# Optimization experiments

Hardware: AMD Instinct MI355X
Metric: run time of the kernel (lower is better)

## Reference

```python
import jax, jax.numpy as jnp
import numpy as np

N_NODES = 100000
N_FEAT = 512
HIDDEN = 128
N_CLASS = 16
N_EDGES = 3200000
ALPHA = 0.25
N_ITERS = 2


def setup_inputs() -> dict:
    key = jax.random.key(0)
    k1, k2, k3, k4, k5 = jax.random.split(key, 5)
    x = jax.random.normal(k1, (N_NODES, N_FEAT), dtype=jnp.float32)
    W1 = jax.random.normal(k2, (N_FEAT, HIDDEN), dtype=jnp.float32) * 0.05
    W2 = jax.random.normal(k3, (HIDDEN, N_CLASS), dtype=jnp.float32) * 0.05
    edge_src = jax.random.randint(k4, (N_EDGES,), 0, N_NODES, dtype=jnp.int32)
    edge_dst = jax.random.randint(k5, (N_EDGES,), 0, N_NODES, dtype=jnp.int32)
    return {"x": x, "W1": W1, "W2": W2, "edge_src": edge_src, "edge_dst": edge_dst}


def reference(x, W1, W2, edge_src, edge_dst):
    # 2-layer GCN features
    hidden_1 = jax.nn.relu(x @ W1)                       # [N, H]
    local_logits = hidden_1 @ W2                         # [N, C]
    # degree of each row of adj (unit edge weights)
    deg = jax.ops.segment_sum(
        jnp.ones_like(edge_src, dtype=x.dtype), edge_src, num_segments=N_NODES
    )                                                    # [N]
    scale = (1.0 - ALPHA) / jnp.maximum(deg, 1e-12)      # [N]
    logits = local_logits
    for _ in range(N_ITERS):
        # SpMM: (adj @ logits)[i] = sum_{(i,j) in E} logits[j]
        agg = jax.ops.segment_sum(logits[edge_dst], edge_src, num_segments=N_NODES)
        logits = scale[:, None] * agg + ALPHA * local_logits
    return jax.nn.log_softmax(logits, axis=1)
```

## Files before the change

### kernel.cpp

```cpp
#include <hip/hip_runtime.h>
#include <math.h>

#define N_NODES 100000
#define N_FEAT  512
#define HIDDEN  128
#define N_CLASS 16
#define N_EDGES 3200000
#define ALPHA   0.25f

#define NB   782
#define CAP  5120
#define TILE 8192
#define NTB  391

typedef __attribute__((ext_vector_type(8))) short short8;
typedef __attribute__((ext_vector_type(4))) float float4v;
typedef __attribute__((ext_vector_type(4))) unsigned uint4v;
typedef __attribute__((ext_vector_type(4))) int int4v;

__device__ inline short f2b(float f) {
    union { float f; unsigned u; } c; c.f = f;
    unsigned r = c.u + 0x7FFF + ((c.u >> 16) & 1);
    return (short)(r >> 16);
}

__device__ __forceinline__ void async_copy16(void* l, const void* g) {
    __builtin_amdgcn_global_load_lds(
        (const __attribute__((address_space(1))) void*)g,
        (__attribute__((address_space(3))) void*)l, 16, 0, 0);
}

__global__ void prep_kernel(const float* __restrict__ W1, const float* __restrict__ W2,
                            short* __restrict__ W1t, short* __restrict__ W2t,
                            int* __restrict__ cursor) {
    int t = blockIdx.x * 256 + threadIdx.x;
    if (t < N_FEAT * HIDDEN) {
        int k = t & 511, n = t >> 9;
        W1t[t] = f2b(W1[(size_t)k * HIDDEN + n]);
    }
    int t2 = t - N_FEAT * HIDDEN;
    if (t2 >= 0 && t2 < HIDDEN * N_CLASS) {
        int k = t2 & 127, n = t2 >> 7;
        W2t[t2] = f2b(W2[(size_t)k * N_CLASS + n]);
    }
    if (t < NB) cursor[t] = t * CAP;
}

__global__ __launch_bounds__(256) void mlp_mfma(const float* __restrict__ x,
                                                const short* __restrict__ W1t,
                                                const short* __restrict__ W2t,
                                                float* __restrict__ local_out,
                                                unsigned short* __restrict__ Lbf) {
    __shared__ __align__(16) char uS[34816];
    __shared__ __align__(16) short W2ts[16 * 136];

    float* const Asf = (float*)uS;
    short* const Bt  = (short*)(uS + 16384);
    short* const Hs  = (short*)uS;

    const int tid  = threadIdx.x;
    const int wave = tid >> 6;
    const int wl   = tid & 63;
    const int lane15 = wl & 15;
    const int quad   = wl >> 4;
    const long block_row = (long)blockIdx.x * 128;

    {
        int n = tid >> 4, koff = (tid & 15) * 8;
        *(short8*)&W2ts[n * 136 + koff] = *(const short8*)&W2t[n * 128 + koff];
    }

    float4v acc[4][4];
#pragma unroll
    for (int i = 0; i < 4; ++i)
#pragma unroll
        for (int j = 0; j < 4; ++j) acc[i][j] = (float4v){0.f, 0.f, 0.f, 0.f};

    const int wr0 = (wave >> 1) * 64;
    const int wc0 = (wave & 1) * 64;

    const int a_rsub = wl >> 3;
    const int a_cch  = (wl & 7) ^ a_rsub;
    const int b_rsub = wl >> 2;
    const int b_cch  = (wl & 3) ^ ((wl >> 3) & 3);
    char* const aBase = uS + wave * 4096;
    char* const bBase = uS + 16384 + wave * 2048;

    const int r7 = lane15 & 7;
    const int rb = (lane15 >> 1) & 3;

    for (int k0 = 0; k0 < N_FEAT; k0 += 32) {
#pragma unroll
        for (int c = 0; c < 4; ++c) {
            long gr = block_row + wave * 32 + c * 8 + a_rsub;
            if (gr > N_NODES - 1) gr = N_NODES - 1;
            async_copy16(aBase + c * 1024, x + gr * N_FEAT + k0 + a_cch * 4);
        }
#pragma unroll
        for (int c = 0; c < 2; ++c) {
            int rr = wave * 32 + c * 16 + b_rsub;
            async_copy16(bBase + c * 1024, W1t + rr * 512 + k0 + b_cch * 8);
        }
        __syncthreads();

        short8 af[4], bfr[4];
#pragma unroll
        for (int i = 0; i < 4; ++i) {
            const float* pa = Asf + (wr0 + i * 16 + lane15) * 32;
            float4 va = *(const float4*)(pa + (((2 * quad) ^ r7) << 2));
            float4 vb = *(const float4*)(pa + (((2 * quad + 1) ^ r7) << 2));
            short8 h;
            h[0] = f2b(va.x); h[1] = f2b(va.y); h[2] = f2b(va.z); h[3] = f2b(va.w);
            h[4] = f2b(vb.x); h[5] = f2b(vb.y); h[6] = f2b(vb.z); h[7] = f2b(vb.w);
            af[i] = h;
        }
#pragma unroll
        for (int j = 0; j < 4; ++j) {
            const short* pb = Bt + (wc0 + j * 16 + lane15) * 32;
            bfr[j] = *(const short8*)(pb + ((quad ^ rb) << 3));
        }
#pragma unroll
        for (int i = 0; i < 4; ++i)
#pragma unroll
            for (int j = 0; j < 4; ++j)
                acc[i][j] = __builtin_amdgcn_mfma_f32_16x16x32_bf16(af[i], bfr[j], acc[i][j], 0, 0, 0);
        __syncthreads();
    }

#pragma unroll
    for (int i = 0; i < 4; ++i)
#pragma unroll
        for (int j = 0; j < 4; ++j)
#pragma unroll
            for (int r = 0; r < 4; ++r) {
                int row = wr0 + i * 16 + quad * 4 + r;
                int colh = wc0 + j * 16 + lane15;
                Hs[row * 136 + colh] = f2b(fmaxf(acc[i][j][r], 0.f));
            }
    __syncthreads();

    float4v acc2[2];
    acc2[0] = (float4v){0.f, 0.f, 0.f, 0.f};
    acc2[1] = acc2[0];
#pragma unroll
    for (int ks = 0; ks < 4; ++ks) {
        short8 a0 = *(short8*)&Hs[(wave * 32 + lane15) * 136 + ks * 32 + quad * 8];
        short8 a1 = *(short8*)&Hs[(wave * 32 + 16 + lane15) * 136 + ks * 32 + quad * 8];
        short8 b  = *(short8*)&W2ts[lane15 * 136 + ks * 32 + quad * 8];
        acc2[0] = __builtin_amdgcn_mfma_f32_16x16x32_bf16(a0, b, acc2[0], 0, 0, 0);
        acc2[1] = __builtin_amdgcn_mfma_f32_16x16x32_bf16(a1, b, acc2[1], 0, 0, 0);
    }
#pragma unroll
    for (int i2 = 0; i2 < 2; ++i2)
#pragma unroll
        for (int r = 0; r < 4; ++r) {
            long grow = block_row + wave * 32 + i2 * 16 + quad * 4 + r;
            if (grow < N_NODES) {
                float v = acc2[i2][r];
                local_out[grow * N_CLASS + lane15] = v;
                Lbf[grow * N_CLASS + lane15] = (unsigned short)f2b(v);
            }
        }
}

__global__ __launch_bounds__(256) void partition_kernel(const int* __restrict__ src,
                                                        const int* __restrict__ dst,
                                                        int* __restrict__ cursor,
                                                        unsigned* __restrict__ bbuf) {
    __shared__ unsigned sbuf[TILE];
    __shared__ unsigned short sbkt[TILE];
    __shared__ int cnt[1024];
    __shared__ int off[1024];
    __shared__ int gbase[NB];
    __shared__ int psum[256];

    const int tid = threadIdx.x;
    const int e0 = blockIdx.x * TILE;
    int n = N_EDGES - e0; if (n > TILE) n = TILE;

    for (int i = tid; i < 1024; i += 256) cnt[i] = 0;
    __syncthreads();

    unsigned pk[32]; int br[32];
#pragma unroll
    for (int k = 0; k < 8; ++k) {
        int i0 = k * 1024 + tid * 4;
        if (i0 < n) {
            int4v s4 = __builtin_nontemporal_load((const int4v*)&src[e0 + i0]);
            int4v d4 = __builtin_nontemporal_load((const int4v*)&dst[e0 + i0]);
#pragma unroll
            for (int j = 0; j < 4; ++j) {
                int s = s4[j], d = d4[j];
                int b = s >> 7;
                int r = atomicAdd(&cnt[b], 1);
                pk[k * 4 + j] = ((unsigned)(s & 127) << 17) | (unsigned)d;
                br[k * 4 + j] = (b << 13) | r;
            }
        } else {
#pragma unroll
            for (int j = 0; j < 4; ++j) br[k * 4 + j] = -1;
        }
    }
    __syncthreads();

    int b4 = tid * 4;
    int c0 = cnt[b4], c1 = cnt[b4 + 1], c2 = cnt[b4 + 2], c3 = cnt[b4 + 3];
    int tsum = c0 + c1 + c2 + c3;
    psum[tid] = tsum;
    __syncthreads();
    for (int o = 1; o < 256; o <<= 1) {
        int t = (tid >= o) ? psum[tid - o] : 0;
        __syncthreads();
        psum[tid] += t;
        __syncthreads();
    }
    int run = psum[tid] - tsum;
    off[b4] = run; off[b4 + 1] = run + c0;
    off[b4 + 2] = run + c0 + c1; off[b4 + 3] = run + c0 + c1 + c2;
    __syncthreads();

    for (int b = tid; b < NB; b += 256) {
        int c = cnt[b];
        if (c > 0) gbase[b] = atomicAdd(&cursor[b], c);
    }

#pragma unroll
    for (int k = 0; k < 32; ++k) {
        if (br[k] >= 0) {
            int b = br[k] >> 13, r = br[k] & 8191;
            int slot = off[b] + r;
            sbuf[slot] = pk[k];
            sbkt[slot] = (unsigned short)b;
        }
    }
    __syncthreads();

    for (int i = tid; i < n; i += 256) {
        int b = sbkt[i];
        __builtin_nontemporal_store(sbuf[i], &bbuf[gbase[b] + (i - off[b])]);
    }
}

__global__ __launch_bounds__(512) void bucket_sort(unsigned* __restrict__ bbuf,
                                                   const int* __restrict__ cursor,
                                                   int* __restrict__ row_start,
                                                   int* __restrict__ row_end,
                                                   float* __restrict__ scale) {
    __shared__ unsigned ein[CAP];
    __shared__ unsigned eout[CAP];
    __shared__ int cnt[128], ssc[128], cur[128];

    const int b = blockIdx.x;
    const int tid = threadIdx.x;
    const int base = b * CAP;
    int n = cursor[b] - base; if (n > CAP) n = CAP;

    for (int i = tid; i < n; i += 512) ein[i] = __builtin_nontemporal_load(&bbuf[base + i]);
    if (tid < 128) cnt[tid] = 0;
    __syncthreads();

    for (int i = tid; i < n; i += 512) atomicAdd(&cnt[ein[i] >> 17], 1);
    __syncthreads();

    int v = (tid < 128) ? cnt[tid] : 0;
    if (tid < 128) ssc[tid] = v;
    __syncthreads();
    for (int o = 1; o < 128; o <<= 1) {
        int t = (tid >= o && tid < 128) ? ssc[tid - o] : 0;
        __syncthreads();
        if (tid < 128) ssc[tid] += t;
        __syncthreads();
    }
    if (tid < 128) cur[tid] = ssc[tid] - v;
    __syncthreads();

    for (int i = tid; i < n; i += 512) {
        unsigned u = ein[i];
        int r = atomicAdd(&cur[u >> 17], 1);
        eout[r] = u & 0x1FFFFu;
    }
    __syncthreads();

    for (int i = tid; i < n; i += 512) __builtin_nontemporal_store(eout[i], &bbuf[base + i]);

    if (tid < 128) {
        int node = (b << 7) + tid;
        if (node < N_NODES) {
            int st = base + ssc[tid] - v;
            row_start[node] = st;
            row_end[node]   = st + v;
            scale[node] = (1.0f - ALPHA) / fmaxf((float)v, 1e-12f);
        }
    }
}

template <int PASS>
__global__ __launch_bounds__(512) void spmm_csr(const unsigned* __restrict__ col,
                                                const int* __restrict__ row_start,
                                                const int* __restrict__ row_end,
                                                const float* __restrict__ scale,
                                                const unsigned short* __restrict__ Ltab,
                                                const float* __restrict__ local,
                                                unsigned short* __restrict__ out_bf,
                                                float* __restrict__ out_f32) {
    int t = blockIdx.x * 512 + threadIdx.x;
    int node = t >> 1;
    int half = t & 1;
    if (node >= N_NODES) return;
    const int rs = row_start[node], re = row_end[node];

    float acc[8];
#pragma unroll
    for (int k = 0; k < 8; ++k) acc[k] = 0.f;

    for (int base = rs & ~3; base < re; base += 16) {
        const uint4v q0 = __builtin_nontemporal_load((const uint4v*)&col[base]);
        const uint4v q1 = __builtin_nontemporal_load((const uint4v*)&col[base + 4]);
        const uint4v q2 = __builtin_nontemporal_load((const uint4v*)&col[base + 8]);
        const uint4v q3 = __builtin_nontemporal_load((const uint4v*)&col[base + 12]);
        int cc[16];
        cc[0]  = (int)q0[0]; cc[1]  = (int)q0[1]; cc[2]  = (int)q0[2]; cc[3]  = (int)q0[3];
        cc[4]  = (int)q1[0]; cc[5]  = (int)q1[1]; cc[6]  = (int)q1[2]; cc[7]  = (int)q1[3];
        cc[8]  = (int)q2[0]; cc[9]  = (int)q2[1]; cc[10] = (int)q2[2]; cc[11] = (int)q2[3];
        cc[12] = (int)q3[0]; cc[13] = (int)q3[1]; cc[14] = (int)q3[2]; cc[15] = (int)q3[3];
#pragma unroll
        for (int j = 0; j < 16; ++j) {
            int idx = base + j;
            if (idx < rs || idx >= re) cc[j] = -1;
        }
        uint4 g[16];
#pragma unroll
        for (int j = 0; j < 16; ++j) {
            int c = (cc[j] < 0) ? 0 : cc[j];
            g[j] = *(const uint4*)&Ltab[(size_t)c * N_CLASS + half * 8];
        }
#pragma unroll
        for (int j = 0; j < 16; ++j) {
            if (cc[j] >= 0) {
                union { unsigned u; float f; } w;
                w.u = g[j].x << 16;          acc[0] += w.f;
                w.u = g[j].x & 0xFFFF0000u;  acc[1] += w.f;
                w.u = g[j].y << 16;          acc[2] += w.f;
                w.u = g[j].y & 0xFFFF0000u;  acc[3] += w.f;
                w.u = g[j].z << 16;          acc[4] += w.f;
                w.u = g[j].z & 0xFFFF0000u;  acc[5] += w.f;
                w.u = g[j].w << 16;          acc[6] += w.f;
                w.u = g[j].w & 0xFFFF0000u;  acc[7] += w.f;
            }
        }
    }

    const float sc = scale[node];
    const float* lp = &local[(size_t)node * N_CLASS + half * 8];
    float4v l0 = __builtin_nontemporal_load((const float4v*)lp);
    float4v l1 = __builtin_nontemporal_load((const float4v*)(lp + 4));
    float r[8];
    r[0] = sc * acc[0] + ALPHA * l0[0]; r[1] = sc * acc[1] + ALPHA * l0[1];
    r[2] = sc * acc[2] + ALPHA * l0[2]; r[3] = sc * acc[3] + ALPHA * l0[3];
    r[4] = sc * acc[4] + ALPHA * l1[0]; r[5] = sc * acc[5] + ALPHA * l1[1];
    r[6] = sc * acc[6] + ALPHA * l1[2]; r[7] = sc * acc[7] + ALPHA * l1[3];

    if (PASS == 1) {
        uint4v o;
        o[0] = ((unsigned)(unsigned short)f2b(r[1]) << 16) | (unsigned)(unsigned short)f2b(r[0]);
        o[1] = ((unsigned)(unsigned short)f2b(r[3]) << 16) | (unsigned)(unsigned short)f2b(r[2]);
        o[2] = ((unsigned)(unsigned short)f2b(r[5]) << 16) | (unsigned)(unsigned short)f2b(r[4]);
        o[3] = ((unsigned)(unsigned short)f2b(r[7]) << 16) | (unsigned)(unsigned short)f2b(r[6]);
        __builtin_nontemporal_store(o, (uint4v*)&out_bf[(size_t)node * N_CLASS + half * 8]);
    } else {
        float mx = r[0];
#pragma unroll
        for (int k = 1; k < 8; ++k) mx = fmaxf(mx, r[k]);
        mx = fmaxf(mx, __shfl_xor(mx, 1));
        float sm = 0.f;
#pragma unroll
        for (int k = 0; k < 8; ++k) sm += expf(r[k] - mx);
        sm += __shfl_xor(sm, 1);
        float ls = logf(sm) + mx;
        float4v o0 = {r[0] - ls, r[1] - ls, r[2] - ls, r[3] - ls};
        float4v o1 = {r[4] - ls, r[5] - ls, r[6] - ls, r[7] - ls};
        float* op = &out_f32[(size_t)node * N_CLASS + half * 8];
        __builtin_nontemporal_store(o0, (float4v*)op);
        __builtin_nontemporal_store(o1, (float4v*)(op + 4));
    }
}

extern "C" void kernel_launch(void* const* d_in, const int* in_sizes, int n_in,
                              void* d_out, int out_size, void* d_ws, size_t ws_size,
                              hipStream_t stream) {
    const float* x    = (const float*)d_in[0];
    const float* W1   = (const float*)d_in[1];
    const float* W2   = (const float*)d_in[2];
    const int*   esrc = (const int*)d_in[3];
    const int*   edst = (const int*)d_in[4];
    float* out = (float*)d_out;
    char*  ws  = (char*)d_ws;

    float*          local   = (float*)         (ws + 0);
    unsigned short* Lbf     = (unsigned short*)(ws + 6400000);
    unsigned short* P1bf    = (unsigned short*)(ws + 9600000);
    float*          scale   = (float*)         (ws + 12800000);
    int*            rstart  = (int*)           (ws + 13200000);
    int*            rend    = (int*)           (ws + 13600000);
    short*          W1t     = (short*)         (ws + 14000000);
    short*          W2t     = (short*)         (ws + 14131072);
    int*            cursor  = (int*)           (ws + 14135168);
    unsigned*       bbuf    = (unsigned*)      (ws + 14138368);

    prep_kernel<<<(N_FEAT * HIDDEN + HIDDEN * N_CLASS + 255) / 256, 256, 0, stream>>>(W1, W2, W1t, W2t, cursor);
    mlp_mfma<<<(N_NODES + 127) / 128, 256, 0, stream>>>(x, W1t, W2t, local, Lbf);

    partition_kernel<<<NTB, 256, 0, stream>>>(esrc, edst, cursor, bbuf);
    bucket_sort<<<NB, 512, 0, stream>>>(bbuf, cursor, rstart, rend, scale);

    const int sgrid = (N_NODES * 2 + 511) / 512;
    spmm_csr<1><<<sgrid, 512, 0, stream>>>(bbuf, rstart, rend, scale, Lbf,  local, P1bf, nullptr);
    spmm_csr<2><<<sgrid, 512, 0, stream>>>(bbuf, rstart, rend, scale, P1bf, local, nullptr, out);
}
```

Measured before the change: 423.3 us.

## Fuse first SpMM pass into bucket sort and split edges across four threads per node

```diff
diff --git a/kernel.cpp b/kernel.cpp
--- a/kernel.cpp
+++ b/kernel.cpp
@@ -237,15 +237,18 @@
 
     for (int i = tid; i < n; i += 256) {
         int b = sbkt[i];
-        __builtin_nontemporal_store(sbuf[i], &bbuf[gbase[b] + (i - off[b])]);
-    }
-}
-
-__global__ __launch_bounds__(512) void bucket_sort(unsigned* __restrict__ bbuf,
-                                                   const int* __restrict__ cursor,
-                                                   int* __restrict__ row_start,
-                                                   int* __restrict__ row_end,
-                                                   float* __restrict__ scale) {
+        bbuf[gbase[b] + (i - off[b])] = sbuf[i];
+    }
+}
+
+__global__ __launch_bounds__(512) void bucket_sort_spmm(unsigned* __restrict__ bbuf,
+                                                        const int* __restrict__ cursor,
+                                                        int* __restrict__ row_start,
+                                                        int* __restrict__ row_end,
+                                                        float* __restrict__ scale,
+                                                        const unsigned short* __restrict__ Ltab,
+                                                        const float* __restrict__ local,
+                                                        unsigned short* __restrict__ P1bf) {
     __shared__ unsigned ein[CAP];
     __shared__ unsigned eout[CAP];
     __shared__ int cnt[128], ssc[128], cur[128];
@@ -281,8 +284,7 @@
     }
     __syncthreads();
 
-    for (int i = tid; i < n; i += 512) __builtin_nontemporal_store(eout[i], &bbuf[base + i]);
-
+    for (int i = tid; i < n; i += 512) bbuf[base + i] = eout[i];
     if (tid < 128) {
         int node = (b << 7) + tid;
         if (node < N_NODES) {
@@ -292,50 +294,34 @@
             scale[node] = (1.0f - ALPHA) / fmaxf((float)v, 1e-12f);
         }
     }
-}
-
-template <int PASS>
-__global__ __launch_bounds__(512) void spmm_csr(const unsigned* __restrict__ col,
-                                                const int* __restrict__ row_start,
-                                                const int* __restrict__ row_end,
-                                                const float* __restrict__ scale,
-                                                const unsigned short* __restrict__ Ltab,
-                                                const float* __restrict__ local,
-                                                unsigned short* __restrict__ out_bf,
-                                                float* __restrict__ out_f32) {
-    int t = blockIdx.x * 512 + threadIdx.x;
-    int node = t >> 1;
-    int half = t & 1;
-    if (node >= N_NODES) return;
-    const int rs = row_start[node], re = row_end[node];
+
+    const int slot = tid >> 2;
+    const int sub  = tid & 3;
+    const int half = sub & 1;
+    const int par  = sub >> 1;
+    const int node = (b << 7) + slot;
+    const int re_l = ssc[slot];
+    const int rs_l = re_l - cnt[slot];
 
     float acc[8];
 #pragma unroll
     for (int k = 0; k < 8; ++k) acc[k] = 0.f;
 
-    for (int base = rs & ~3; base < re; base += 16) {
-        const uint4v q0 = __builtin_nontemporal_load((const uint4v*)&col[base]);
-        const uint4v q1 = __builtin_nontemporal_load((const uint4v*)&col[base + 4]);
-        const uint4v q2 = __builtin_nontemporal_load((const uint4v*)&col[base + 8]);
-        const uint4v q3 = __builtin_nontemporal_load((const uint4v*)&col[base + 12]);
-        int cc[16];
-        cc[0]  = (int)q0[0]; cc[1]  = (int)q0[1]; cc[2]  = (int)q0[2]; cc[3]  = (int)q0[3];
-        cc[4]  = (int)q1[0]; cc[5]  = (int)q1[1]; cc[6]  = (int)q1[2]; cc[7]  = (int)q1[3];
-        cc[8]  = (int)q2[0]; cc[9]  = (int)q2[1]; cc[10] = (int)q2[2]; cc[11] = (int)q2[3];
-        cc[12] = (int)q3[0]; cc[13] = (int)q3[1]; cc[14] = (int)q3[2]; cc[15] = (int)q3[3];
-#pragma unroll
-        for (int j = 0; j < 16; ++j) {
-            int idx = base + j;
-            if (idx < rs || idx >= re) cc[j] = -1;
-        }
-        uint4 g[16];
-#pragma unroll
-        for (int j = 0; j < 16; ++j) {
+    for (int b0 = rs_l; b0 < re_l; b0 += 16) {
+        int cc[8];
+#pragma unroll
+        for (int j = 0; j < 8; ++j) {
+            int e = b0 + 2 * j + par;
+            cc[j] = (e < re_l) ? (int)eout[e] : -1;
+        }
+        uint4 g[8];
+#pragma unroll
+        for (int j = 0; j < 8; ++j) {
             int c = (cc[j] < 0) ? 0 : cc[j];
             g[j] = *(const uint4*)&Ltab[(size_t)c * N_CLASS + half * 8];
         }
 #pragma unroll
-        for (int j = 0; j < 16; ++j) {
+        for (int j = 0; j < 8; ++j) {
             if (cc[j] >= 0) {
                 union { unsigned u; float f; } w;
                 w.u = g[j].x << 16;          acc[0] += w.f;
@@ -349,25 +335,99 @@
             }
         }
     }
-
-    const float sc = scale[node];
-    const float* lp = &local[(size_t)node * N_CLASS + half * 8];
-    float4v l0 = __builtin_nontemporal_load((const float4v*)lp);
-    float4v l1 = __builtin_nontemporal_load((const float4v*)(lp + 4));
-    float r[8];
-    r[0] = sc * acc[0] + ALPHA * l0[0]; r[1] = sc * acc[1] + ALPHA * l0[1];
-    r[2] = sc * acc[2] + ALPHA * l0[2]; r[3] = sc * acc[3] + ALPHA * l0[3];
-    r[4] = sc * acc[4] + ALPHA * l1[0]; r[5] = sc * acc[5] + ALPHA * l1[1];
-    r[6] = sc * acc[6] + ALPHA * l1[2]; r[7] = sc * acc[7] + ALPHA * l1[3];
-
-    if (PASS == 1) {
+#pragma unroll
+    for (int k = 0; k < 8; ++k) acc[k] += __shfl_xor(acc[k], 2);
+
+    if (par == 0 && node < N_NODES) {
+        const float sc = (1.0f - ALPHA) / fmaxf((float)cnt[slot], 1e-12f);
+        const float* lp = &local[(size_t)node * N_CLASS + half * 8];
+        float4v l0 = __builtin_nontemporal_load((const float4v*)lp);
+        float4v l1 = __builtin_nontemporal_load((const float4v*)(lp + 4));
+        float r[8];
+        r[0] = sc * acc[0] + ALPHA * l0[0]; r[1] = sc * acc[1] + ALPHA * l0[1];
+        r[2] = sc * acc[2] + ALPHA * l0[2]; r[3] = sc * acc[3] + ALPHA * l0[3];
+        r[4] = sc * acc[4] + ALPHA * l1[0]; r[5] = sc * acc[5] + ALPHA * l1[1];
+        r[6] = sc * acc[6] + ALPHA * l1[2]; r[7] = sc * acc[7] + ALPHA * l1[3];
         uint4v o;
         o[0] = ((unsigned)(unsigned short)f2b(r[1]) << 16) | (unsigned)(unsigned short)f2b(r[0]);
         o[1] = ((unsigned)(unsigned short)f2b(r[3]) << 16) | (unsigned)(unsigned short)f2b(r[2]);
         o[2] = ((unsigned)(unsigned short)f2b(r[5]) << 16) | (unsigned)(unsigned short)f2b(r[4]);
         o[3] = ((unsigned)(unsigned short)f2b(r[7]) << 16) | (unsigned)(unsigned short)f2b(r[6]);
-        __builtin_nontemporal_store(o, (uint4v*)&out_bf[(size_t)node * N_CLASS + half * 8]);
-    } else {
+        *(uint4v*)&P1bf[(size_t)node * N_CLASS + half * 8] = o;
+    }
+}
+
+__global__ __launch_bounds__(512) void spmm_pass2(const unsigned* __restrict__ col,
+                                                  const int* __restrict__ row_start,
+                                                  const int* __restrict__ row_end,
+                                                  const float* __restrict__ scale,
+                                                  const unsigned short* __restrict__ Ltab,
+                                                  const float* __restrict__ local,
+                                                  float* __restrict__ out_f32) {
+    int t = blockIdx.x * 512 + threadIdx.x;
+    int node = t >> 2;
+    if (node >= N_NODES) return;
+    const int sub  = t & 3;
+    const int half = sub & 1;
+    const int par  = sub >> 1;
+    const int rs = row_start[node], re = row_end[node];
+
+    float acc[8];
+#pragma unroll
+    for (int k = 0; k < 8; ++k) acc[k] = 0.f;
+
+    for (int b0 = rs & ~3; b0 < re; b0 += 16) {
+        const uint4v q0 = __builtin_nontemporal_load((const uint4v*)&col[b0]);
+        const uint4v q1 = __builtin_nontemporal_load((const uint4v*)&col[b0 + 4]);
+        const uint4v q2 = __builtin_nontemporal_load((const uint4v*)&col[b0 + 8]);
+        const uint4v q3 = __builtin_nontemporal_load((const uint4v*)&col[b0 + 12]);
+        unsigned ce[8];
+        ce[0] = par ? q0[1] : q0[0];  ce[1] = par ? q0[3] : q0[2];
+        ce[2] = par ? q1[1] : q1[0];  ce[3] = par ? q1[3] : q1[2];
+        ce[4] = par ? q2[1] : q2[0];  ce[5] = par ? q2[3] : q2[2];
+        int cc[8];
+        unsigned ce6 = par ? q3[1] : q3[0], ce7 = par ? q3[3] : q3[2];
+        ce[6] = ce6; ce[7] = ce7;
+#pragma unroll
+        for (int j = 0; j < 8; ++j) {
+            int e = b0 + 2 * j + par;
+            cc[j] = (e >= rs && e < re) ? (int)ce[j] : -1;
+        }
+        uint4 g[8];
+#pragma unroll
+        for (int j = 0; j < 8; ++j) {
+            int c = (cc[j] < 0) ? 0 : cc[j];
+            g[j] = *(const uint4*)&Ltab[(size_t)c * N_CLASS + half * 8];
+        }
+#pragma unroll
+        for (int j = 0; j < 8; ++j) {
+            if (cc[j] >= 0) {
+                union { unsigned u; float f; } w;
+                w.u = g[j].x << 16;          acc[0] += w.f;
+                w.u = g[j].x & 0xFFFF0000u;  acc[1] += w.f;
+                w.u = g[j].y << 16;          acc[2] += w.f;
+                w.u = g[j].y & 0xFFFF0000u;  acc[3] += w.f;
+                w.u = g[j].z << 16;          acc[4] += w.f;
+                w.u = g[j].z & 0xFFFF0000u;  acc[5] += w.f;
+                w.u = g[j].w << 16;          acc[6] += w.f;
+                w.u = g[j].w & 0xFFFF0000u;  acc[7] += w.f;
+            }
+        }
+    }
+#pragma unroll
+    for (int k = 0; k < 8; ++k) acc[k] += __shfl_xor(acc[k], 2);
+
+    if (par == 0) {
+        const float sc = scale[node];
+        const float* lp = &local[(size_t)node * N_CLASS + half * 8];
+        float4v l0 = __builtin_nontemporal_load((const float4v*)lp);
+        float4v l1 = __builtin_nontemporal_load((const float4v*)(lp + 4));
+        float r[8];
+        r[0] = sc * acc[0] + ALPHA * l0[0]; r[1] = sc * acc[1] + ALPHA * l0[1];
+        r[2] = sc * acc[2] + ALPHA * l0[2]; r[3] = sc * acc[3] + ALPHA * l0[3];
+        r[4] = sc * acc[4] + ALPHA * l1[0]; r[5] = sc * acc[5] + ALPHA * l1[1];
+        r[6] = sc * acc[6] + ALPHA * l1[2]; r[7] = sc * acc[7] + ALPHA * l1[3];
+
         float mx = r[0];
 #pragma unroll
         for (int k = 1; k < 8; ++k) mx = fmaxf(mx, r[k]);
@@ -411,9 +471,8 @@
     mlp_mfma<<<(N_NODES + 127) / 128, 256, 0, stream>>>(x, W1t, W2t, local, Lbf);
 
     partition_kernel<<<NTB, 256, 0, stream>>>(esrc, edst, cursor, bbuf);
-    bucket_sort<<<NB, 512, 0, stream>>>(bbuf, cursor, rstart, rend, scale);
-
-    const int sgrid = (N_NODES * 2 + 511) / 512;
-    spmm_csr<1><<<sgrid, 512, 0, stream>>>(bbuf, rstart, rend, scale, Lbf,  local, P1bf, nullptr);
-    spmm_csr<2><<<sgrid, 512, 0, stream>>>(bbuf, rstart, rend, scale, P1bf, local, nullptr, out);
-}
+    bucket_sort_spmm<<<NB, 512, 0, stream>>>(bbuf, cursor, rstart, rend, scale, Lbf, local, P1bf);
+
+    const int p2grid = (N_NODES * 4 + 511) / 512;
+    spmm_pass2<<<p2grid, 512, 0, stream>>>(bbuf, rstart, rend, scale, P1bf, local, out);
+}
```

Result: faster. 397.2 us (-6.2%).
